# Kernel tuning notes

Measured on AMD Instinct MI355X. Metric: run time of the kernel, lower is better.

Reference implementation:

```python
import jax, jax.numpy as jnp
import numpy as np

N_NEG = 60
TEMP = 0.07

def _normalize(x, axis):
    n = jnp.sqrt(jnp.sum(x * x, axis=axis, keepdims=True))
    return x / jnp.maximum(n, 1e-12)

def _grid_sample(img, grid):
    # img [B,C,H,W], grid [B,h,w,2] in [-1,1]; bilinear, padding_mode='border', align_corners=False
    B, C, H, W = img.shape
    ix = jnp.clip((grid[..., 0] + 1.0) * (W * 0.5) - 0.5, 0.0, W - 1.0)
    iy = jnp.clip((grid[..., 1] + 1.0) * (H * 0.5) - 0.5, 0.0, H - 1.0)
    x0 = jnp.floor(ix); y0 = jnp.floor(iy)
    x1 = jnp.minimum(x0 + 1.0, W - 1.0); y1 = jnp.minimum(y0 + 1.0, H - 1.0)
    wx = (ix - x0)[:, None]; wy = (iy - y0)[:, None]  # [B,1,h,w]
    imgf = img.reshape(B, C, H * W)
    hh, ww = grid.shape[1], grid.shape[2]
    def gat(yy, xx):
        idx = (yy * W + xx).astype(jnp.int32).reshape(B, 1, hh * ww)
        return jnp.take_along_axis(imgf, idx, axis=2).reshape(B, C, hh, ww)
    v00 = gat(y0, x0); v01 = gat(y0, x1); v10 = gat(y1, x0); v11 = gat(y1, x1)
    return (v00 * (1 - wx) * (1 - wy) + v01 * wx * (1 - wy)
            + v10 * (1 - wx) * wy + v11 * wx * wy)

def _forward(ref_fms, tgt_fms, target_l, target_r, queue):
    b, c, h, w = ref_fms.shape
    s = target_l.shape[-1] // w  # integer downscale factor (nearest interpolate == strided slice)
    disps_l = target_l[:, :, ::s, ::s] / float(s)   # [b,1,h,w]
    disps_r = target_r[:, :, ::s, ::s] / float(s)
    xb = jnp.broadcast_to(jnp.linspace(0.0, 1.0, w), (b, h, w))
    yb = jnp.broadcast_to(jnp.linspace(0.0, 1.0, h)[:, None], (b, h, w))

    def warp(img, disp):
        g = jnp.stack([xb + disp[:, 0] / w, yb], axis=-1)
        return _grid_sample(img, 2.0 * g - 1.0)

    # occlusion / validity mask (detached in the original)
    index = jnp.broadcast_to(jnp.arange(w, dtype=ref_fms.dtype), (b, 1, h, w))
    l2r2l = warp(warp(index, disps_r), -disps_l)
    masko = jnp.abs(index - l2r2l)[:, 0] < 3.0
    mask = masko & (disps_l[:, 0] > 0.0) & (xb - disps_l[:, 0] / w >= 0.0)
    mask = jax.lax.stop_gradient(mask).astype(ref_fms.dtype)  # [b,h,w]

    query = _normalize(ref_fms, 1)
    # positive: warp right feature to left view via disparity
    gpos = jnp.stack([xb - disps_l[:, 0] / w, yb], axis=-1)
    positive = _normalize(_grid_sample(tgt_fms, 2.0 * gpos - 1.0), 1)
    l_pos = jnp.einsum('bchw,bchw->bhw', query, positive)[..., None]

    # negatives: random integer pixel shifts around positive location
    # (no n_neg-fold repeat of tgt_fms; vmap grid_sample over the n axis instead)
    k1, k2 = jax.random.split(jax.random.key(1234))
    mag = jax.random.randint(k1, (b, h, w, N_NEG), 1, 25).astype(ref_fms.dtype)
    sgn = jnp.sign(jax.random.uniform(k2, (b, h, w, N_NEG)) - 0.5).astype(ref_fms.dtype)
    x_right = (xb - disps_l[:, 0] / w) * w
    fx = jnp.mod(x_right[..., None] + mag * sgn, float(w)) / w
    fy = fx / h  # faithful to original code (y coord reuses the normalized x coord)
    grids = jnp.moveaxis(jnp.stack([fx, fy], axis=-1), 3, 0)  # [n,b,h,w,2]
    neg = jax.vmap(lambda g: _grid_sample(tgt_fms, 2.0 * g - 1.0))(grids)  # [n,b,c,h,w]
    neg = _normalize(jnp.moveaxis(neg, 0, -1), 1)  # [b,c,h,w,n]
    l_neg = jnp.einsum('bchw,bchwn->bhwn', query, neg)

    qn = _normalize(queue, 0)  # forward re-normalizes the queue each call
    l_q = jnp.einsum('bchw,ck->bhwk', query, jax.lax.stop_gradient(qn))

    logits = jnp.concatenate([l_pos, l_neg, l_q], axis=-1) * mask[..., None]
    logits = logits.reshape(b * h * w, -1) / TEMP
    # CrossEntropyLoss with all-zero labels (positive is class 0)
    return jnp.mean(-jax.nn.log_softmax(logits, axis=-1)[:, 0])

def setup_inputs():
    key = jax.random.key(0)
    k1, k2, k3, k4, k5 = jax.random.split(key, 5)
    b, c, h, w = 2, 128, 64, 128
    H, W = 4 * h, 4 * w
    return {
        'ref_fms': jax.random.normal(k1, (b, c, h, w), jnp.float32),
        'tgt_fms': jax.random.normal(k2, (b, c, h, w), jnp.float32),
        'target_l': jax.random.uniform(k3, (b, 1, H, W), jnp.float32) * 64.0,
        'target_r': jax.random.uniform(k4, (b, 1, H, W), jnp.float32) * 64.0,
        'queue': jax.random.normal(k5, (c, 6000), jnp.float32),
    }

def reference(ref_fms, tgt_fms, target_l, target_r, queue):
    return _forward(ref_fms, tgt_fms, target_l, target_r, queue)
```

## Files before the change

kernel.cpp:

```cpp
#include <hip/hip_runtime.h>
#include <stdint.h>
#include <math.h>

#define HFM 64
#define WFM 128
#define CFM 128
#define BN 2
#define HWFM (HFM*WFM)
#define NPIX (BN*HWFM)
#define KQ 6000
#define KQP 6144
#define NNEG 60
#define NE (NPIX*NNEG)
#define EHALF_U 491520u
#define MSHIFT 15.0f
#define LOG2E 1.4426950408889634f
#define BSTRIDE 136

typedef _Float16 f16_8 __attribute__((ext_vector_type(8)));
typedef _Float16 f16_2 __attribute__((ext_vector_type(2)));
typedef float f32_4 __attribute__((ext_vector_type(4)));

__host__ __device__ __forceinline__ void threefry2x32(uint32_t k0, uint32_t k1,
                                                      uint32_t x0, uint32_t x1,
                                                      uint32_t* o0, uint32_t* o1) {
  uint32_t ks2 = k0 ^ k1 ^ 0x1BD11BDAu;
  x0 += k0; x1 += k1;
#define TFR(r) { x0 += x1; x1 = (x1 << (r)) | (x1 >> (32 - (r))); x1 ^= x0; }
  TFR(13) TFR(15) TFR(26) TFR(6)
  x0 += k1;  x1 += ks2 + 1u;
  TFR(17) TFR(29) TFR(16) TFR(24)
  x0 += ks2; x1 += k0 + 2u;
  TFR(13) TFR(15) TFR(26) TFR(6)
  x0 += k0;  x1 += k1 + 3u;
  TFR(17) TFR(29) TFR(16) TFR(24)
  x0 += k1;  x1 += ks2 + 4u;
  TFR(13) TFR(15) TFR(26) TFR(6)
  x0 += ks2; x1 += k0 + 5u;
#undef TFR
  *o0 = x0; *o1 = x1;
}

__device__ __forceinline__ void gs_coord(float t, float halfdim, float maxc,
                                         int* i0, int* i1, float* w) {
  float g = 2.0f * t - 1.0f;
  float x = (g + 1.0f) * halfdim - 0.5f;
  x = fminf(fmaxf(x, 0.0f), maxc);
  float f = floorf(x);
  *i0 = (int)f;
  *w = x - f;
  *i1 = (int)fminf(f + 1.0f, maxc);
}

__global__ __launch_bounds__(256) void k_A(
    const float* __restrict__ ref, const float* __restrict__ tgt,
    const float* __restrict__ queue,
    const float* __restrict__ target_l, const float* __restrict__ target_r,
    _Float16* __restrict__ refTf, _Float16* __restrict__ tgtTf,
    _Float16* __restrict__ queueTf, float2* __restrict__ qeb,
    float* __restrict__ maskArr, float* __restrict__ xr) {
  __shared__ float tile[32][33];
  int blk = blockIdx.x;
  int tid = threadIdx.x;
  if (blk < 64) {
    int p = blk * 256 + tid;
    int b = p >> 13;
    int rem = p & (HWFM - 1);
    int i = rem >> 7, j = rem & 127;
    const float stepx = 1.0f / 127.0f, stepy = 1.0f / 63.0f;
    float xb = (j == 127) ? 1.0f : j * stepx;
    float yb = (i == 63) ? 1.0f : i * stepy;
    const float* tl = target_l + (size_t)b * 256 * 512;
    const float* tr = target_r + (size_t)b * 256 * 512;
    float dl = tl[(4 * i) * 512 + 4 * j] * 0.25f;
    int y0i, y1i; float wy;
    gs_coord(yb, 32.0f, 63.0f, &y0i, &y1i, &wy);
    float t = xb - dl * (1.0f / 128.0f);
    int x0i, x1i; float wx;
    gs_coord(t, 64.0f, 127.0f, &x0i, &x1i, &wx);
    auto innerv = [&](int y, int x) -> float {
      float xbx = (x == 127) ? 1.0f : x * stepx;
      float drv = tr[(4 * y) * 512 + 4 * x] * 0.25f;
      float ti = xbx + drv * (1.0f / 128.0f);
      float g = 2.0f * ti - 1.0f;
      float ix2 = fminf(fmaxf((g + 1.0f) * 64.0f - 0.5f, 0.0f), 127.0f);
      float x0f = floorf(ix2);
      float wxp = ix2 - x0f;
      float x1f = fminf(x0f + 1.0f, 127.0f);
      return x0f * (1.0f - wxp) + x1f * wxp;
    };
    float v00 = innerv(y0i, x0i), v01 = innerv(y0i, x1i);
    float v10 = innerv(y1i, x0i), v11 = innerv(y1i, x1i);
    float l2r2l = v00 * (1.0f - wx) * (1.0f - wy) + v01 * wx * (1.0f - wy)
                + v10 * (1.0f - wx) * wy + v11 * wx * wy;
    bool masko = fabsf((float)j - l2r2l) < 3.0f;
    bool mk = masko && (dl > 0.0f) && (t >= 0.0f);
    maskArr[p] = mk ? 1.0f : 0.0f;
    xr[p] = t * 128.0f;
  } else if (blk < 88) {
    int k = (blk - 64) * 256 + tid;
    if (k < KQP) {
      if (k >= KQ) { qeb[k] = make_float2(0.0f, -1000.0f); }
      else {
        float ss = 0.0f;
        for (int c = 0; c < CFM; c++) { float v = queue[c * KQ + k]; ss += v * v; }
        float qi = 1.0f / fmaxf(sqrtf(ss), 1e-12f);
        qeb[k] = make_float2(qi * (LOG2E / 0.07f), -MSHIFT * LOG2E);
      }
    }
  } else if (blk < 856) {
    int q = blk - 88;
    int cy = q / 192, nx = q - cy * 192;
    int n0 = nx * 32, c0 = cy * 32;
    int tx = tid & 31, ty = tid >> 5;
#pragma unroll
    for (int i = 0; i < 32; i += 8) {
      int n = n0 + tx;
      tile[ty + i][tx] = (n < KQ) ? queue[(size_t)(c0 + ty + i) * KQ + n] : 0.0f;
    }
    __syncthreads();
#pragma unroll
    for (int i = 0; i < 32; i += 8)
      queueTf[(size_t)(n0 + ty + i) * CFM + (c0 + tx)] = (_Float16)tile[tx][ty + i];
  } else {
    int fblk = blk - 856;
    int z = fblk >> 10, yb_ = (fblk >> 8) & 3, xb_ = fblk & 255;
    int arr = z >> 1, b = z & 1;
    const float* src = (arr == 0 ? ref : tgt) + (size_t)b * CFM * HWFM;
    _Float16* dst = (arr == 0 ? refTf : tgtTf) + (size_t)b * HWFM * CFM;
    int x0 = xb_ * 32, y0 = yb_ * 32;
    int tx = tid & 31, ty = tid >> 5;
#pragma unroll
    for (int i = 0; i < 32; i += 8)
      tile[ty + i][tx] = src[(size_t)(y0 + ty + i) * HWFM + x0 + tx];
    __syncthreads();
#pragma unroll
    for (int i = 0; i < 32; i += 8)
      dst[(size_t)(x0 + ty + i) * CFM + (y0 + tx)] = (_Float16)tile[tx][ty + i];
  }
}

__global__ __launch_bounds__(256) void k_compact(const float* __restrict__ maskArr,
                                                 int* __restrict__ count,
                                                 int* __restrict__ list) {
  __shared__ int wsum[4];
  int tid = threadIdx.x;
  int lane = tid & 63, wave = tid >> 6;
  int base_p = tid * 64;
  unsigned long long bits = 0ull;
  const float4* m4 = (const float4*)(maskArr + base_p);
#pragma unroll
  for (int k = 0; k < 16; k++) {
    float4 v = m4[k];
    if (v.x > 0.0f) bits |= 1ull << (4 * k + 0);
    if (v.y > 0.0f) bits |= 1ull << (4 * k + 1);
    if (v.z > 0.0f) bits |= 1ull << (4 * k + 2);
    if (v.w > 0.0f) bits |= 1ull << (4 * k + 3);
  }
  int m = __popcll(bits);
  int scan = m;
#pragma unroll
  for (int off = 1; off < 64; off <<= 1) {
    int n = __shfl_up(scan, off, 64);
    if (lane >= off) scan += n;
  }
  if (lane == 63) wsum[wave] = scan;
  __syncthreads();
  int wbase = 0;
  for (int w = 0; w < wave; w++) wbase += wsum[w];
  int idx = wbase + scan - m;
  for (int k = 0; k < 64; k++) {
    if ((bits >> k) & 1ull) list[idx++] = base_p + k;
  }
  if (tid == 255) *count = idx;
}

__global__ __launch_bounds__(256) void k_B(
    const _Float16* __restrict__ refTf, const _Float16* __restrict__ tgtTf,
    _Float16* __restrict__ QTfc, float* __restrict__ stats,
    const float* __restrict__ xr,
    float* __restrict__ S, float* __restrict__ logit0,
    const int* __restrict__ count, const int* __restrict__ list) {
  int blk = blockIdx.x;
  int tid = threadIdx.x;
  int lane = tid & 63;
  if (blk < 64) {
    int sub = tid >> 6;
    int xg = blk * 4 + sub;
    int b = xg >> 7, x = xg & 127;
    int xp = min(x + 1, 127);
    int c2 = lane * 2;
    int base = b * HWFM;
    f16_2 c0  = *(const f16_2*)(tgtTf + (size_t)(base + x) * CFM + c2);
    f16_2 c1  = *(const f16_2*)(tgtTf + (size_t)(base + WFM + x) * CFM + c2);
    f16_2 c0p = *(const f16_2*)(tgtTf + (size_t)(base + xp) * CFM + c2);
    f16_2 c1p = *(const f16_2*)(tgtTf + (size_t)(base + WFM + xp) * CFM + c2);
    float a0 = (float)c0[0], a1 = (float)c0[1];
    float b0 = (float)c1[0], b1 = (float)c1[1];
    float p0 = (float)c0p[0], p1 = (float)c0p[1];
    float q0 = (float)c1p[0], q1 = (float)c1p[1];
    float s[7];
    s[0] = a0 * a0 + a1 * a1;
    s[1] = a0 * b0 + a1 * b1;
    s[2] = b0 * b0 + b1 * b1;
    s[3] = a0 * p0 + a1 * p1;
    s[4] = a0 * q0 + a1 * q1;
    s[5] = b0 * p0 + b1 * p1;
    s[6] = b0 * q0 + b1 * q1;
#pragma unroll
    for (int o = 32; o; o >>= 1)
#pragma unroll
      for (int k = 0; k < 7; k++) s[k] += __shfl_xor(s[k], o, 64);
    if (lane == 0) {
      float* st = stats + (size_t)xg * 8;
#pragma unroll
      for (int k = 0; k < 7; k++) st[k] = s[k];
      st[7] = 0.0f;
    }
  } else {
    int wave = tid >> 6;
    int cnt = *count;
    int slot = (blk - 64) * 4 + wave;
    if (slot >= cnt) return;
    int p = list[slot];
    int b = p >> 13;
    int rem = p & (HWFM - 1);
    int i = rem >> 7;
    const float stepy = 1.0f / 63.0f;
    float yb = (i == 63) ? 1.0f : i * stepy;
    float t = xr[p] * (1.0f / 128.0f);
    int y0i, y1i; float wy;
    gs_coord(yb, 32.0f, 63.0f, &y0i, &y1i, &wy);
    int x0i, x1i; float wx;
    gs_coord(t, 64.0f, 127.0f, &x0i, &x1i, &wx);

    int c2 = lane * 2;
    f16_2 q2 = *(const f16_2*)(refTf + (size_t)p * CFM + c2);
    int bo = b * HWFM;
    f16_2 a2 = *(const f16_2*)(tgtTf + (size_t)(bo + y0i * WFM + x0i) * CFM + c2);
    f16_2 b2 = *(const f16_2*)(tgtTf + (size_t)(bo + y0i * WFM + x1i) * CFM + c2);
    f16_2 cc2 = *(const f16_2*)(tgtTf + (size_t)(bo + y1i * WFM + x0i) * CFM + c2);
    f16_2 d2 = *(const f16_2*)(tgtTf + (size_t)(bo + y1i * WFM + x1i) * CFM + c2);

    float w00 = (1.0f - wx) * (1.0f - wy), w01 = wx * (1.0f - wy);
    float w10 = (1.0f - wx) * wy,          w11 = wx * wy;
    float q0 = (float)q2[0], q1 = (float)q2[1];
    float v0 = w00 * (float)a2[0] + w01 * (float)b2[0] + w10 * (float)cc2[0] + w11 * (float)d2[0];
    float v1 = w00 * (float)a2[1] + w01 * (float)b2[1] + w10 * (float)cc2[1] + w11 * (float)d2[1];

    float s0 = q0 * q0 + q1 * q1;
    float s1 = q0 * v0 + q1 * v1;
    float s2 = v0 * v0 + v1 * v1;
#pragma unroll
    for (int o = 32; o; o >>= 1) {
      s0 += __shfl_xor(s0, o, 64);
      s1 += __shfl_xor(s1, o, 64);
      s2 += __shfl_xor(s2, o, 64);
    }
    float inv = 1.0f / fmaxf(sqrtf(s0), 1e-12f);
    f16_2 qw; qw[0] = (_Float16)(q0 * inv); qw[1] = (_Float16)(q1 * inv);
    *(f16_2*)(QTfc + (size_t)slot * CFM + c2) = qw;
    if (lane == 0) {
      float lpos = (s1 * inv) / fmaxf(sqrtf(s2), 1e-12f);
      float lg0 = lpos / 0.07f;
      logit0[p] = lg0;
      S[p] = expf(lg0 - MSHIFT);
    }
  }
}

__global__ __launch_bounds__(256) void k_gemm(
    const _Float16* __restrict__ QTfc,
    const _Float16* __restrict__ queueTf,
    const _Float16* __restrict__ tgtTf,
    const float2* __restrict__ qeb,
    float* __restrict__ S, _Float16* __restrict__ Dh,
    const int* __restrict__ count, const int* __restrict__ list) {
  __shared__ _Float16 Bs[128 * BSTRIDE];
  __shared__ float Srow[64];
  __shared__ int pb[64];
  int tid = threadIdx.x;
  int cnt = *count;
  int pblk = blockIdx.y * 64;
  if (pblk >= cnt) return;
  int wave = tid >> 6, lane = tid & 63;
  int quad = lane >> 4, l16 = lane & 15;
  int wm = wave >> 1, wn = wave & 1;

  if (tid < 64) {
    Srow[tid] = 0.0f;
    pb[tid] = list[min(pblk + tid, cnt - 1)] >> 13;
  }

  f16_8 Af[2][4];
  int r0 = pblk + wm * 32;
#pragma unroll
  for (int mt = 0; mt < 2; mt++) {
    const _Float16* arow = QTfc + (size_t)min(r0 + mt * 16 + l16, cnt - 1) * CFM + quad * 8;
#pragma unroll
    for (int ks = 0; ks < 4; ks++)
      Af[mt][ks] = *(const f16_8*)(arow + ks * 32);
  }

  f16_8 sreg[8];
  int srow[8], sc16[8];
#pragma unroll
  for (int it = 0; it < 8; it++) {
    int idx = it * 256 + tid;
    srow[it] = idx >> 4; sc16[it] = idx & 15;
  }
  auto load_src = [&](const _Float16* bsrc) {
#pragma unroll
    for (int it = 0; it < 8; it++)
      sreg[it] = *(const f16_8*)(bsrc + (size_t)srow[it] * CFM + sc16[it] * 8);
  };
  auto write_lds = [&]() {
#pragma unroll
    for (int it = 0; it < 8; it++)
      *(f16_8*)(&Bs[srow[it] * BSTRIDE + sc16[it] * 8]) = sreg[it];
  };

  int nbase = blockIdx.x * 4 * 128;
  bool hasD = blockIdx.x < 4;
  float rowsum[2][4] = {{0.0f,0.0f,0.0f,0.0f},{0.0f,0.0f,0.0f,0.0f}};

  if (hasD) {
    int batch = blockIdx.x >> 1;
    load_src(tgtTf + ((size_t)batch * HWFM + (blockIdx.x & 1) * 128) * CFM);
  } else {
    load_src(queueTf + (size_t)nbase * CFM);
  }

  if (hasD) {
    write_lds();
    __syncthreads();
    load_src(queueTf + (size_t)nbase * CFM);
    int batch = blockIdx.x >> 1;
    f32_4 acc[2][4];
#pragma unroll
    for (int mt = 0; mt < 2; mt++)
#pragma unroll
      for (int nt = 0; nt < 4; nt++)
        acc[mt][nt] = (f32_4){0.0f, 0.0f, 0.0f, 0.0f};
#pragma unroll
    for (int ks = 0; ks < 4; ks++) {
      f16_8 Bk[4];
#pragma unroll
      for (int nt = 0; nt < 4; nt++)
        Bk[nt] = *(const f16_8*)(&Bs[(wn * 64 + nt * 16 + l16) * BSTRIDE + ks * 32 + quad * 8]);
#pragma unroll
      for (int mt = 0; mt < 2; mt++)
#pragma unroll
        for (int nt = 0; nt < 4; nt++)
          acc[mt][nt] = __builtin_amdgcn_mfma_f32_16x16x32_f16(Af[mt][ks], Bk[nt], acc[mt][nt], 0, 0, 0);
    }
#pragma unroll
    for (int mt = 0; mt < 2; mt++)
#pragma unroll
      for (int nt = 0; nt < 4; nt++)
#pragma unroll
        for (int r = 0; r < 4; r++) {
          int rowloc = wm * 32 + mt * 16 + quad * 4 + r;
          int slot = pblk + rowloc;
          int colL = (blockIdx.x & 1) * 128 + wn * 64 + nt * 16 + l16;
          if (slot < cnt && pb[rowloc] == batch)
            Dh[(size_t)slot * 256 + colL] = (_Float16)acc[mt][nt][r];
        }
    __syncthreads();
  }

#pragma unroll
  for (int ic = 0; ic < 4; ic++) {
    int n0 = nbase + ic * 128;
    write_lds();
    __syncthreads();
    if (ic < 3) load_src(queueTf + (size_t)(n0 + 128) * CFM);
    float2 qb[4];
#pragma unroll
    for (int nt = 0; nt < 4; nt++) qb[nt] = qeb[n0 + wn * 64 + nt * 16 + l16];

    f32_4 acc[2][4];
#pragma unroll
    for (int mt = 0; mt < 2; mt++)
#pragma unroll
      for (int nt = 0; nt < 4; nt++)
        acc[mt][nt] = (f32_4){0.0f, 0.0f, 0.0f, 0.0f};
#pragma unroll
    for (int ks = 0; ks < 4; ks++) {
      f16_8 Bk[4];
#pragma unroll
      for (int nt = 0; nt < 4; nt++)
        Bk[nt] = *(const f16_8*)(&Bs[(wn * 64 + nt * 16 + l16) * BSTRIDE + ks * 32 + quad * 8]);
#pragma unroll
      for (int mt = 0; mt < 2; mt++)
#pragma unroll
        for (int nt = 0; nt < 4; nt++)
          acc[mt][nt] = __builtin_amdgcn_mfma_f32_16x16x32_f16(Af[mt][ks], Bk[nt], acc[mt][nt], 0, 0, 0);
    }
#pragma unroll
    for (int nt = 0; nt < 4; nt++)
#pragma unroll
      for (int mt = 0; mt < 2; mt++)
#pragma unroll
        for (int r = 0; r < 4; r++)
          rowsum[mt][r] += exp2f(fmaf(acc[mt][nt][r], qb[nt].x, qb[nt].y));
    __syncthreads();
  }

#pragma unroll
  for (int mt = 0; mt < 2; mt++)
#pragma unroll
    for (int r = 0; r < 4; r++) {
      float vv = rowsum[mt][r];
      vv += __shfl_xor(vv, 1);
      vv += __shfl_xor(vv, 2);
      vv += __shfl_xor(vv, 4);
      vv += __shfl_xor(vv, 8);
      rowsum[mt][r] = vv;
    }
  if (l16 == 0) {
#pragma unroll
    for (int mt = 0; mt < 2; mt++)
#pragma unroll
      for (int r = 0; r < 4; r++)
        atomicAdd(&Srow[wm * 32 + mt * 16 + quad * 4 + r], rowsum[mt][r]);
  }
  __syncthreads();
  if (tid < 64) {
    int pr = pblk + tid;
    if (pr < cnt) atomicAdd(&S[list[pr]], Srow[tid]);
  }
}

__global__ __launch_bounds__(256) void k_negatives_lite(
    const _Float16* __restrict__ Dh, const float* __restrict__ stats,
    const float* __restrict__ xr, float* __restrict__ S,
    const int* __restrict__ count, const int* __restrict__ list,
    uint32_t k1a, uint32_t k1b, uint32_t k2a, uint32_t k2b) {
  int tid = threadIdx.x;
  int wave = tid >> 6, lane = tid & 63;
  int cnt = *count;
  int slot = blockIdx.x * 4 + wave;
  if (slot >= cnt) return;
  int p = list[slot];
  int b = p >> 13;
  float esum = 0.0f;
  if (lane < NNEG) {
    uint32_t e = (uint32_t)(p * NNEG + lane);
    uint32_t h0, h1;
    threefry2x32(k1a, k1b, e, e + (uint32_t)NE, &h0, &h1);
    uint32_t off = ((h0 % 24u) * 16u + (h1 % 24u)) % 24u;
    float mag = (float)(1u + off);
    uint32_t ub;
    {
      uint32_t a, bm;
      if (e < EHALF_U) { threefry2x32(k2a, k2b, e, e + EHALF_U, &a, &bm); ub = a; }
      else             { threefry2x32(k2a, k2b, e - EHALF_U, e, &a, &bm); ub = bm; }
    }
    float u = __uint_as_float((ub >> 9) | 0x3F800000u) - 1.0f;
    float sg = (u > 0.5f) ? 1.0f : ((u < 0.5f) ? -1.0f : 0.0f);

    float v = xr[p] + mag * sg;
    float r = fmodf(v, 128.0f);
    if (r < 0.0f) r += 128.0f;
    float fx = r * (1.0f / 128.0f);
    float fy = fx * (1.0f / 64.0f);
    int x0i, x1i, y0i, y1i; float wx, wy;
    gs_coord(fx, 64.0f, 127.0f, &x0i, &x1i, &wx);
    gs_coord(fy, 32.0f, 63.0f, &y0i, &y1i, &wy);

    const _Float16* Dp = Dh + (size_t)slot * 256;
    float d00 = (float)Dp[x0i], d01 = (float)Dp[x1i];
    float d10 = (float)Dp[128 + x0i], d11 = (float)Dp[128 + x1i];
    float u0 = 1.0f - wy, u1 = wy;
    float dv0 = u0 * d00 + u1 * d10;
    float dv1 = u0 * d01 + u1 * d11;
    float dot = (1.0f - wx) * dv0 + wx * dv1;

    const float* st0 = stats + (size_t)(b * 128 + x0i) * 8;
    const float* st1 = stats + (size_t)(b * 128 + x1i) * 8;
    float4 sa = *(const float4*)st0;
    float4 sb = *(const float4*)(st0 + 4);
    float4 sc = *(const float4*)st1;
    float a0 = u0 * u0, a1 = u0 * u1, a2 = u1 * u1;
    float nB0 = a0 * sa.x + 2.0f * a1 * sa.y + a2 * sa.z;
    float nB1 = a0 * sc.x + 2.0f * a1 * sc.y + a2 * sc.z;
    float cB  = a0 * sa.w + a1 * (sb.x + sb.y) + a2 * sb.z;
    float wx0 = 1.0f - wx;
    float nsq = wx0 * wx0 * nB0 + 2.0f * wx * wx0 * cB + wx * wx * nB1;
    float ln = dot / fmaxf(sqrtf(fmaxf(nsq, 0.0f)), 1e-12f);
    esum = __expf(ln * (1.0f / 0.07f) - MSHIFT);
  }
#pragma unroll
  for (int o = 32; o; o >>= 1) esum += __shfl_xor(esum, o, 64);
  if (lane == 0) atomicAdd(&S[p], esum);
}

__global__ __launch_bounds__(1024) void k_finalize(
    const float* __restrict__ S, const float* __restrict__ logit0,
    const float* __restrict__ maskArr, float* __restrict__ out) {
  int tid = threadIdx.x;
  const float cmask = logf(6061.0f);
  double acc = 0.0;
  for (int p = tid; p < NPIX; p += 1024) {
    float term = (maskArr[p] > 0.0f) ? (logf(S[p]) + MSHIFT - logit0[p]) : cmask;
    acc += (double)term;
  }
#pragma unroll
  for (int off = 32; off; off >>= 1) acc += __shfl_down(acc, off, 64);
  __shared__ double sd[16];
  if ((tid & 63) == 0) sd[tid >> 6] = acc;
  __syncthreads();
  if (tid == 0) {
    double tot = 0.0;
    for (int w = 0; w < 16; w++) tot += sd[w];
    out[0] = (float)(tot / (double)NPIX);
  }
}

extern "C" void kernel_launch(void* const* d_in, const int* in_sizes, int n_in,
                              void* d_out, int out_size, void* d_ws, size_t ws_size,
                              hipStream_t stream) {
  const float* ref   = (const float*)d_in[0];
  const float* tgt   = (const float*)d_in[1];
  const float* tl    = (const float*)d_in[2];
  const float* tr    = (const float*)d_in[3];
  const float* queue = (const float*)d_in[4];
  float* out = (float*)d_out;
  float* ws = (float*)d_ws;

  float2* qeb = (float2*)ws;
  float* S    = ws + 12288;
  float* lg0  = ws + 28672;
  float* mk   = ws + 45056;
  float* xr   = ws + 61440;
  int* count  = (int*)(ws + 77824);
  int* list   = (int*)(ws + 77840);
  _Float16* QTfc    = (_Float16*)(ws + 94464);
  _Float16* queueTf = (_Float16*)(ws + 1143040);
  _Float16* tgtTf   = (_Float16*)(ws + 1536256);
  _Float16* refTf   = (_Float16*)(ws + 2584832);
  float* stats = ws + 3633408;
  _Float16* Dh = (_Float16*)(ws + 3635456);

  uint32_t b0o0, b0o1, b1o0, b1o1;
  threefry2x32(0u, 1234u, 0u, 2u, &b0o0, &b0o1);
  threefry2x32(0u, 1234u, 1u, 3u, &b1o0, &b1o1);
  uint32_t k1a = b0o0, k1b = b1o0, k2a = b0o1, k2b = b1o1;

  k_A<<<dim3(4952), dim3(256), 0, stream>>>(ref, tgt, queue, tl, tr,
                                            refTf, tgtTf, queueTf, qeb, mk, xr);
  k_compact<<<dim3(1), dim3(256), 0, stream>>>(mk, count, list);
  k_B<<<dim3(64 + 4096), dim3(256), 0, stream>>>(refTf, tgtTf, QTfc, stats,
                                                 xr, S, lg0, count, list);
  k_gemm<<<dim3(12, NPIX / 64), dim3(256), 0, stream>>>(QTfc, queueTf, tgtTf, qeb,
                                                        S, Dh, count, list);
  k_negatives_lite<<<dim3(NPIX / 4), dim3(256), 0, stream>>>(Dh, stats, xr, S, count, list,
                                                             k1a, k1b, k2a, k2b);
  k_finalize<<<dim3(1), dim3(1024), 0, stream>>>(S, lg0, mk, out);
}
```

Measured before the change: 133.0 us.

## Double-buffer LDS with XOR swizzle and double per-block queue chunks in GEMM

The queue GEMM kernel now uses two LDS buffers, so the next B tile is written into the spare buffer during compute and only one barrier is needed per iteration. Padding is replaced by an XOR swizzle of 16-byte columns to avoid bank conflicts. Each block now handles 8 chunks of 128 queue columns instead of 4, halving the grid's x dimension. This doubles LDS use per block and lengthens each block's serial work, which may reduce occupancy and parallelism.

```diff
diff --git a/kernel.cpp b/kernel.cpp
--- a/kernel.cpp
+++ b/kernel.cpp
@@ -15,7 +15,7 @@
 #define EHALF_U 491520u
 #define MSHIFT 15.0f
 #define LOG2E 1.4426950408889634f
-#define BSTRIDE 136
+#define BSTRIDE 128
 
 typedef _Float16 f16_8 __attribute__((ext_vector_type(8)));
 typedef _Float16 f16_2 __attribute__((ext_vector_type(2)));
@@ -276,7 +276,7 @@
     const float2* __restrict__ qeb,
     float* __restrict__ S, _Float16* __restrict__ Dh,
     const int* __restrict__ count, const int* __restrict__ list) {
-  __shared__ _Float16 Bs[128 * BSTRIDE];
+  __shared__ _Float16 Bs[2][128 * BSTRIDE];
   __shared__ float Srow[64];
   __shared__ int pb[64];
   int tid = threadIdx.x;
@@ -303,39 +303,43 @@
   }
 
   f16_8 sreg[8];
-  int srow[8], sc16[8];
+  int srow[8], scol[8];
 #pragma unroll
   for (int it = 0; it < 8; it++) {
     int idx = it * 256 + tid;
-    srow[it] = idx >> 4; sc16[it] = idx & 15;
-  }
+    int row = idx >> 4, c16 = idx & 15;
+    srow[it] = row;
+    scol[it] = (c16 ^ (row & 15)) * 8;
+  }
+  int sc16raw[8];
+#pragma unroll
+  for (int it = 0; it < 8; it++) sc16raw[it] = ((it * 256 + tid) & 15) * 8;
+
   auto load_src = [&](const _Float16* bsrc) {
 #pragma unroll
     for (int it = 0; it < 8; it++)
-      sreg[it] = *(const f16_8*)(bsrc + (size_t)srow[it] * CFM + sc16[it] * 8);
+      sreg[it] = *(const f16_8*)(bsrc + (size_t)srow[it] * CFM + sc16raw[it]);
   };
-  auto write_lds = [&]() {
+  auto write_lds = [&](int buf) {
 #pragma unroll
     for (int it = 0; it < 8; it++)
-      *(f16_8*)(&Bs[srow[it] * BSTRIDE + sc16[it] * 8]) = sreg[it];
+      *(f16_8*)(&Bs[buf][srow[it] * BSTRIDE + scol[it]]) = sreg[it];
   };
-
-  int nbase = blockIdx.x * 4 * 128;
-  bool hasD = blockIdx.x < 4;
+  auto read_b = [&](int buf, int rl, int ks) -> f16_8 {
+    int col = ((ks * 4 + quad) ^ (rl & 15)) * 8;
+    return *(const f16_8*)(&Bs[buf][rl * BSTRIDE + col]);
+  };
+
+  int nbase = blockIdx.x * 8 * 128;
+  int cur;
   float rowsum[2][4] = {{0.0f,0.0f,0.0f,0.0f},{0.0f,0.0f,0.0f,0.0f}};
 
-  if (hasD) {
+  if (blockIdx.x < 4) {
     int batch = blockIdx.x >> 1;
     load_src(tgtTf + ((size_t)batch * HWFM + (blockIdx.x & 1) * 128) * CFM);
-  } else {
-    load_src(queueTf + (size_t)nbase * CFM);
-  }
-
-  if (hasD) {
-    write_lds();
+    write_lds(0);
     __syncthreads();
     load_src(queueTf + (size_t)nbase * CFM);
-    int batch = blockIdx.x >> 1;
     f32_4 acc[2][4];
 #pragma unroll
     for (int mt = 0; mt < 2; mt++)
@@ -347,7 +351,7 @@
       f16_8 Bk[4];
 #pragma unroll
       for (int nt = 0; nt < 4; nt++)
-        Bk[nt] = *(const f16_8*)(&Bs[(wn * 64 + nt * 16 + l16) * BSTRIDE + ks * 32 + quad * 8]);
+        Bk[nt] = read_b(0, wn * 64 + nt * 16 + l16, ks);
 #pragma unroll
       for (int mt = 0; mt < 2; mt++)
 #pragma unroll
@@ -366,15 +370,20 @@
           if (slot < cnt && pb[rowloc] == batch)
             Dh[(size_t)slot * 256 + colL] = (_Float16)acc[mt][nt][r];
         }
+    write_lds(1);
     __syncthreads();
-  }
-
-#pragma unroll
-  for (int ic = 0; ic < 4; ic++) {
+    cur = 1;
+  } else {
+    load_src(queueTf + (size_t)nbase * CFM);
+    write_lds(0);
+    __syncthreads();
+    cur = 0;
+  }
+
+#pragma unroll
+  for (int ic = 0; ic < 8; ic++) {
     int n0 = nbase + ic * 128;
-    write_lds();
-    __syncthreads();
-    if (ic < 3) load_src(queueTf + (size_t)(n0 + 128) * CFM);
+    if (ic + 1 < 8) load_src(queueTf + (size_t)(n0 + 128) * CFM);
     float2 qb[4];
 #pragma unroll
     for (int nt = 0; nt < 4; nt++) qb[nt] = qeb[n0 + wn * 64 + nt * 16 + l16];
@@ -390,13 +399,15 @@
       f16_8 Bk[4];
 #pragma unroll
       for (int nt = 0; nt < 4; nt++)
-        Bk[nt] = *(const f16_8*)(&Bs[(wn * 64 + nt * 16 + l16) * BSTRIDE + ks * 32 + quad * 8]);
+        Bk[nt] = read_b(cur, wn * 64 + nt * 16 + l16, ks);
 #pragma unroll
       for (int mt = 0; mt < 2; mt++)
 #pragma unroll
         for (int nt = 0; nt < 4; nt++)
           acc[mt][nt] = __builtin_amdgcn_mfma_f32_16x16x32_f16(Af[mt][ks], Bk[nt], acc[mt][nt], 0, 0, 0);
     }
+    if (ic + 1 < 8) write_lds(cur ^ 1);
+
 #pragma unroll
     for (int nt = 0; nt < 4; nt++)
 #pragma unroll
@@ -405,6 +416,7 @@
         for (int r = 0; r < 4; r++)
           rowsum[mt][r] += exp2f(fmaf(acc[mt][nt][r], qb[nt].x, qb[nt].y));
     __syncthreads();
+    cur ^= 1;
   }
 
 #pragma unroll
@@ -553,8 +565,8 @@
   k_compact<<<dim3(1), dim3(256), 0, stream>>>(mk, count, list);
   k_B<<<dim3(64 + 4096), dim3(256), 0, stream>>>(refTf, tgtTf, QTfc, stats,
                                                  xr, S, lg0, count, list);
-  k_gemm<<<dim3(12, NPIX / 64), dim3(256), 0, stream>>>(QTfc, queueTf, tgtTf, qeb,
-                                                        S, Dh, count, list);
+  k_gemm<<<dim3(6, NPIX / 64), dim3(256), 0, stream>>>(QTfc, queueTf, tgtTf, qeb,
+                                                       S, Dh, count, list);
   k_negatives_lite<<<dim3(NPIX / 4), dim3(256), 0, stream>>>(Dh, stats, xr, S, count, list,
                                                              k1a, k1b, k2a, k2b);
   k_finalize<<<dim3(1), dim3(1024), 0, stream>>>(S, lg0, mk, out);
```

Measured after the change: 132.8 us. About the same (-0.1%).
